# Kernel tuning notes

Measured on AMD Instinct MI355X. Metric: run time of the kernel, lower is better.

## Reference

```python
import jax, jax.numpy as jnp
import numpy as np

B, N, D_NODE, D_EDGE, D_GRAPH = 2, 1024, 128, 16, 128
MID, OUT = 64, 128


def _linear_params(key, fan_in, fan_out):
    # haiku Linear default: truncated-normal(stddev=1/sqrt(fan_in)) weight, zero bias
    w = jax.random.normal(key, (fan_in, fan_out), dtype=jnp.float32) / np.sqrt(fan_in)
    b = jnp.zeros((fan_out,), dtype=jnp.float32)
    return w, b


def setup_inputs() -> dict:
    key = jax.random.key(0)
    ks = jax.random.split(key, 12)
    features = jax.random.normal(ks[0], (B, N, D_NODE), dtype=jnp.float32)
    e_features = jax.random.normal(ks[1], (B, N, N, D_EDGE), dtype=jnp.float32)
    g_features = jax.random.normal(ks[2], (B, D_GRAPH), dtype=jnp.float32)
    adj = jax.random.randint(ks[3], (B, N, N), 0, 2).astype(jnp.float32)
    # ensure self-loops so every row has at least one valid neighbor
    adj = jnp.maximum(adj, jnp.eye(N, dtype=jnp.float32)[None])
    Wm, bm = _linear_params(ks[4], D_NODE, OUT)
    Wskip, bskip = _linear_params(ks[5], D_NODE, OUT)
    W1, b1 = _linear_params(ks[6], D_NODE, MID)
    W2, b2 = _linear_params(ks[7], D_NODE, MID)
    We, be = _linear_params(ks[8], D_EDGE, MID)
    Wg, bg = _linear_params(ks[9], D_GRAPH, MID)
    Wa, ba = _linear_params(ks[10], MID, 1)
    return dict(features=features, e_features=e_features, g_features=g_features,
                adj=adj, Wm=Wm, bm=bm, Wskip=Wskip, bskip=bskip,
                W1=W1, b1=b1, W2=W2, b2=b2, We=We, be=be, Wg=Wg, bg=bg,
                Wa=Wa, ba=ba)


def reference(features, e_features, g_features, adj,
              Wm, bm, Wskip, bskip, W1, b1, W2, b2, We, be, Wg, bg, Wa, ba):
    # bias mask: 0 where edge exists, -1e9 where not
    bias_mat = (adj - 1.0) * 1e9  # (b,n,n)

    values = features @ Wm + bm          # (b,n,out)
    pre_att_1 = features @ W1 + b1       # (b,n,mid) -> per-target j
    pre_att_2 = features @ W2 + b2       # (b,n,mid) -> per-source i
    pre_att_e = e_features @ We + be     # (b,n,n,mid)
    pre_att_g = g_features @ Wg + bg     # (b,mid)

    # pre_att[b,i,j] = p1[b,j] + p2[b,i] + pe[b,i,j] + pg[b]
    pre_att = (pre_att_1[:, None, :, :] + pre_att_2[:, :, None, :]
               + pre_att_e + pre_att_g[:, None, None, :])  # (b,n,n,mid)

    logits = jnp.squeeze(jax.nn.leaky_relu(pre_att) @ Wa + ba, axis=-1)  # (b,n,n)
    coefs = jax.nn.softmax(logits + bias_mat, axis=-1)                   # (b,n,n)

    ret = jnp.matmul(coefs, values)       # (b,n,out)
    ret = ret + (features @ Wskip + bskip)  # residual
    return jax.nn.relu(ret)               # activation=relu
```

## Files before the change

### kernel.cpp

```cpp
#include <hip/hip_runtime.h>
#include <hip/hip_bf16.h>
#include <cstdint>

#define B_   2
#define N_   1024
#define DN_  128
#define DE_  16
#define DG_  128
#define MID_ 64
#define OUT_ 128
#define TI_  2
#define PR_ROWS 4

typedef short bf16x8 __attribute__((ext_vector_type(8)));
typedef float f32x4  __attribute__((ext_vector_type(4)));

__device__ inline short f2bf(float f) {
    union { float f; unsigned u; } v; v.f = f;
    unsigned r = v.u + 0x7FFFu + ((v.u >> 16) & 1u);
    return (short)(unsigned short)(r >> 16);
}

__device__ inline unsigned pk2(float lo, float hi) {
    union { __hip_bfloat162 h; unsigned u; } p;
    p.h = __float22bfloat162_rn(make_float2(lo, hi));
    return p.u;
}

__global__ void __launch_bounds__(384) prep_all(
    const float* __restrict__ features, const float* __restrict__ g_features,
    const float* __restrict__ Wm, const float* __restrict__ bm,
    const float* __restrict__ Wskip, const float* __restrict__ bskip,
    const float* __restrict__ W1, const float* __restrict__ b1,
    const float* __restrict__ W2, const float* __restrict__ b2,
    const float* __restrict__ We, const float* __restrict__ be,
    const float* __restrict__ Wg, const float* __restrict__ bg,
    float* __restrict__ values, float* __restrict__ skipo,
    float* __restrict__ P1x, float* __restrict__ p2,
    float* __restrict__ pg, short* __restrict__ We_frag)
{
    const int t   = threadIdx.x;
    const int blk = blockIdx.x;

    if (blk == 512) {
        for (int e = t; e < 4 * 64 * 8; e += 384) {
            const int c    = e >> 9;
            const int lane = (e >> 3) & 63;
            const int j    = e & 7;
            const int quad = lane >> 4, s = lane & 15;
            short v = 0;
            if (quad < 2) v = f2bf(We[(quad * 8 + j) * MID_ + c * 16 + s]);
            We_frag[e] = v;
        }
        return;
    }
    if (blk == 513) {
        if (t < MID_) {
            float a0 = bg[t], a1 = bg[t];
            for (int k = 0; k < DG_; ++k) {
                const float w = Wg[k * MID_ + t];
                a0 += g_features[k] * w;
                a1 += g_features[DG_ + k] * w;
            }
            pg[t] = a0; pg[MID_ + t] = a1;
        }
        return;
    }

    const int r0 = blk * PR_ROWS;
    __shared__ float feat[PR_ROWS][DN_];
    for (int idx = t; idx < PR_ROWS * DN_; idx += 384)
        feat[idx >> 7][idx & 127] = features[(size_t)r0 * DN_ + idx];
    __syncthreads();

    const float* W; int c, stride; float base; float* outp; int ostride;
    if (t < 128) {
        W = Wm;    c = t;       stride = OUT_; base = bm[c];
        outp = values + (size_t)r0 * OUT_ + c; ostride = OUT_;
    } else if (t < 256) {
        W = Wskip; c = t - 128; stride = OUT_; base = bskip[c];
        outp = skipo + (size_t)r0 * OUT_ + c;  ostride = OUT_;
    } else if (t < 320) {
        W = W1;    c = t - 256; stride = MID_; base = b1[c] + be[c];
        outp = P1x + (size_t)r0 * MID_ + c;    ostride = MID_;
    } else {
        W = W2;    c = t - 320; stride = MID_; base = b2[c];
        outp = p2 + (size_t)r0 * MID_ + c;     ostride = MID_;
    }

    float acc[PR_ROWS] = {};
    for (int k = 0; k < DN_; ++k) {
        const float w = W[k * stride + c];
        #pragma unroll
        for (int q = 0; q < PR_ROWS; ++q) acc[q] += feat[q][k] * w;
    }
    #pragma unroll
    for (int q = 0; q < PR_ROWS; ++q) outp[q * ostride] = acc[q] + base;
}

__global__ void __launch_bounds__(256, 4) gat_main(
    const float* __restrict__ e_features, const float* __restrict__ adj,
    const short* __restrict__ We_frag, const float* __restrict__ Wa,
    const float* __restrict__ values, const float* __restrict__ skipo,
    const float* __restrict__ P1x, const float* __restrict__ p2,
    const float* __restrict__ pg, float* __restrict__ out)
{
    const int t    = threadIdx.x;
    const int wv   = t >> 6;
    const int l    = t & 63;
    const int quad = l >> 4;
    const int s    = l & 15;
    const int r    = blockIdx.x;
    const int b    = (r >> 2) & 1;
    const int i0   = (((r >> 3) << 2) | (r & 3)) * TI_;

    __shared__ float lgP[TI_][N_];
    __shared__ float redv[4][16][20];
    __shared__ float sinv[TI_];
    __shared__ float pmax[4];
    __shared__ float psum[4];

    bf16x8 bfr[4];
    float  wa_r[4], p2i[TI_][4];
    #pragma unroll
    for (int c = 0; c < 4; ++c) {
        bfr[c]  = *(const bf16x8*)&We_frag[(c * 64 + l) * 8];
        wa_r[c] = Wa[c * 16 + s];
        const float pgc = pg[b * MID_ + c * 16 + s];
        #pragma unroll
        for (int ii = 0; ii < TI_; ++ii)
            p2i[ii][c] = p2[((size_t)(b * N_ + i0 + ii)) * MID_ + c * 16 + s] + pgc;
    }
    const size_t erow0 = (size_t)(b * N_ + i0) * N_;

    float4 eA[TI_][2];
    if (quad < 2) {
        #pragma unroll
        for (int ii = 0; ii < TI_; ++ii) {
            const float* ep = &e_features[(erow0 + (size_t)ii * N_ + wv * 16 + s) * DE_ + quad * 8];
            eA[ii][0] = *(const float4*)ep;
            eA[ii][1] = *(const float4*)(ep + 4);
        }
    }
    for (int it = 0; it < 16; ++it) {
        const int tile = wv + it * 4;
        const int j0   = tile * 16;

        unsigned af[TI_][4];
        #pragma unroll
        for (int ii = 0; ii < TI_; ++ii) {
            if (quad < 2) {
                af[ii][0] = pk2(eA[ii][0].x, eA[ii][0].y);
                af[ii][1] = pk2(eA[ii][0].z, eA[ii][0].w);
                af[ii][2] = pk2(eA[ii][1].x, eA[ii][1].y);
                af[ii][3] = pk2(eA[ii][1].z, eA[ii][1].w);
            } else {
                af[ii][0] = af[ii][1] = af[ii][2] = af[ii][3] = 0u;
            }
        }
        if (it < 15) {
            const int jn = (tile + 4) * 16;
            if (quad < 2) {
                #pragma unroll
                for (int ii = 0; ii < TI_; ++ii) {
                    const float* ep = &e_features[(erow0 + (size_t)ii * N_ + jn + s) * DE_ + quad * 8];
                    eA[ii][0] = *(const float4*)ep;
                    eA[ii][1] = *(const float4*)(ep + 4);
                }
            }
        }
        float base[4][4];
        {
            const float* pb = &P1x[((size_t)(b * N_) + j0 + quad * 4) * MID_ + s];
            #pragma unroll
            for (int c = 0; c < 4; ++c)
                #pragma unroll
                for (int rr = 0; rr < 4; ++rr)
                    base[c][rr] = pb[rr * MID_ + c * 16];
        }
        #pragma unroll
        for (int ii = 0; ii < TI_; ++ii) {
            union { unsigned u[4]; bf16x8 v; } a;
            a.u[0] = af[ii][0]; a.u[1] = af[ii][1];
            a.u[2] = af[ii][2]; a.u[3] = af[ii][3];
            f32x4 acc[4];
            #pragma unroll
            for (int c = 0; c < 4; ++c) {
                acc[c] = (f32x4){0.f, 0.f, 0.f, 0.f};
                acc[c] = __builtin_amdgcn_mfma_f32_16x16x32_bf16(a.v, bfr[c], acc[c], 0, 0, 0);
            }
            float tt[4];
            #pragma unroll
            for (int rr = 0; rr < 4; ++rr) {
                float x0 = acc[0][rr] + base[0][rr] + p2i[ii][0];
                float x1 = acc[1][rr] + base[1][rr] + p2i[ii][1];
                float x2 = acc[2][rr] + base[2][rr] + p2i[ii][2];
                float x3 = acc[3][rr] + base[3][rr] + p2i[ii][3];
                x0 = fmaxf(x0, 0.01f * x0);
                x1 = fmaxf(x1, 0.01f * x1);
                x2 = fmaxf(x2, 0.01f * x2);
                x3 = fmaxf(x3, 0.01f * x3);
                tt[rr] = x0 * wa_r[0] + x1 * wa_r[1] + x2 * wa_r[2] + x3 * wa_r[3];
            }
            #pragma unroll
            for (int o = 1; o < 16; o <<= 1) {
                tt[0] += __shfl_xor(tt[0], o);
                tt[1] += __shfl_xor(tt[1], o);
                tt[2] += __shfl_xor(tt[2], o);
                tt[3] += __shfl_xor(tt[3], o);
            }
            if (s < 4) lgP[ii][j0 + quad * 4 + s] = tt[s];
        }
    }
    __syncthreads();

    {
        const int rw = wv & 1, h = wv >> 1;
        const int c0 = h * 512 + l * 4;
        const size_t arb = (size_t)(b * N_ + i0 + rw) * N_;
        float4 lv[2], av[2];
        #pragma unroll
        for (int q = 0; q < 2; ++q) {
            lv[q] = *(const float4*)&lgP[rw][c0 + 256 * q];
            av[q] = *(const float4*)&adj[arb + c0 + 256 * q];
        }
        const float NEG = -3.4e38f;
        float m = NEG;
        #pragma unroll
        for (int q = 0; q < 2; ++q) {
            m = fmaxf(m, av[q].x > 0.f ? lv[q].x : NEG);
            m = fmaxf(m, av[q].y > 0.f ? lv[q].y : NEG);
            m = fmaxf(m, av[q].z > 0.f ? lv[q].z : NEG);
            m = fmaxf(m, av[q].w > 0.f ? lv[q].w : NEG);
        }
        #pragma unroll
        for (int o = 1; o < 64; o <<= 1) m = fmaxf(m, __shfl_xor(m, o));
        if (l == 0) pmax[wv] = m;
        __syncthreads();
        m = fmaxf(pmax[rw], pmax[2 + rw]);
        float sum = 0.f;
        #pragma unroll
        for (int q = 0; q < 2; ++q) {
            float4 e4;
            e4.x = av[q].x > 0.f ? __expf(lv[q].x - m) : 0.f;
            e4.y = av[q].y > 0.f ? __expf(lv[q].y - m) : 0.f;
            e4.z = av[q].z > 0.f ? __expf(lv[q].z - m) : 0.f;
            e4.w = av[q].w > 0.f ? __expf(lv[q].w - m) : 0.f;
            *(float4*)&lgP[rw][c0 + 256 * q] = e4;
            sum += (e4.x + e4.y) + (e4.z + e4.w);
        }
        #pragma unroll
        for (int o = 1; o < 64; o <<= 1) sum += __shfl_xor(sum, o);
        if (l == 0) psum[wv] = sum;
        __syncthreads();
        if (t < TI_) sinv[t] = 1.0f / (psum[t] + psum[t + 2]);
    }

    const int cg = l & 15, jp = l >> 4, ch0 = cg * 8;
    float acc[TI_][8] = {};
    const float* vb = values + (size_t)b * N_ * OUT_ + ch0;
    for (int k = 0; k < 64; ++k) {
        const int j = wv * 4 + jp + k * 16;
        float cw[TI_];
        #pragma unroll
        for (int ii = 0; ii < TI_; ++ii) cw[ii] = lgP[ii][j];
        const float* vp = vb + (size_t)j * OUT_;
        const float4 v0 = *(const float4*)vp;
        const float4 v1 = *(const float4*)(vp + 4);
        const float vv[8] = {v0.x, v0.y, v0.z, v0.w, v1.x, v1.y, v1.z, v1.w};
        #pragma unroll
        for (int ii = 0; ii < TI_; ++ii)
            #pragma unroll
            for (int kk = 0; kk < 8; ++kk)
                acc[ii][kk] += cw[ii] * vv[kk];
    }
    #pragma unroll
    for (int ii = 0; ii < TI_; ++ii)
        #pragma unroll
        for (int kk = 0; kk < 8; ++kk) {
            acc[ii][kk] += __shfl_xor(acc[ii][kk], 16);
            acc[ii][kk] += __shfl_xor(acc[ii][kk], 32);
        }
    if (l < 16) {
        #pragma unroll
        for (int ii = 0; ii < TI_; ++ii)
            #pragma unroll
            for (int q = 0; q < 2; ++q) {
                float4 w4 = make_float4(acc[ii][q * 4], acc[ii][q * 4 + 1],
                                        acc[ii][q * 4 + 2], acc[ii][q * 4 + 3]);
                *(float4*)&redv[wv][l][ii * 8 + q * 4] = w4;
            }
    }
    __syncthreads();
    {
        const int ch = t & 127, g = ch >> 3, kk = ch & 7;
        const int ii = t >> 7;
        float sum = redv[0][g][ii * 8 + kk];
        #pragma unroll
        for (int w = 1; w < 4; ++w) sum += redv[w][g][ii * 8 + kk];
        const size_t ob = ((size_t)(b * N_ + i0 + ii)) * OUT_ + ch;
        out[ob] = fmaxf(sum * sinv[ii] + skipo[ob], 0.f);
    }
}

extern "C" void kernel_launch(void* const* d_in, const int* in_sizes, int n_in,
                              void* d_out, int out_size, void* d_ws, size_t ws_size,
                              hipStream_t stream) {
    const float* features   = (const float*)d_in[0];
    const float* e_features = (const float*)d_in[1];
    const float* g_features = (const float*)d_in[2];
    const float* adj        = (const float*)d_in[3];
    const float* Wm    = (const float*)d_in[4];
    const float* bm    = (const float*)d_in[5];
    const float* Wskip = (const float*)d_in[6];
    const float* bskip = (const float*)d_in[7];
    const float* W1    = (const float*)d_in[8];
    const float* b1    = (const float*)d_in[9];
    const float* W2    = (const float*)d_in[10];
    const float* b2    = (const float*)d_in[11];
    const float* We    = (const float*)d_in[12];
    const float* be    = (const float*)d_in[13];
    const float* Wg    = (const float*)d_in[14];
    const float* bg    = (const float*)d_in[15];
    const float* Wa    = (const float*)d_in[16];
    float* out = (float*)d_out;

    float* ws      = (float*)d_ws;
    float* values  = ws;
    float* skipo   = ws + 262144;
    float* P1x     = ws + 524288;
    float* p2      = ws + 655360;
    float* pg      = ws + 786432;
    short* We_frag = (short*)(ws + 786560);

    prep_all<<<B_ * N_ / PR_ROWS + 2, 384, 0, stream>>>(
        features, g_features, Wm, bm, Wskip, bskip, W1, b1, W2, b2,
        We, be, Wg, bg, values, skipo, P1x, p2, pg, We_frag);
    gat_main<<<B_ * N_ / TI_, 256, 0, stream>>>(
        e_features, adj, We_frag, Wa, values, skipo, P1x, p2, pg, out);
}
```

Baseline: 290.3 us.

## Split fused GAT kernel into logits and attention kernels with doubled grid

The single fused kernel becomes two. A logits kernel, launched with twice as many blocks each covering half the j range, writes the attention logits to a global workspace. A separate attention kernel then reads them back for the softmax and the aggregation. The bias sum (P1 + p2 + pg) is also folded into the MFMA accumulator input, which removes the post-MFMA adds. The aim is more parallelism and occupancy on the e_features-bound phase, at the cost of an extra launch and an 8 MB round trip of logits through global memory.

```diff
diff --git a/kernel.cpp b/kernel.cpp
--- a/kernel.cpp
+++ b/kernel.cpp
@@ -98,12 +98,11 @@
     for (int q = 0; q < PR_ROWS; ++q) outp[q * ostride] = acc[q] + base;
 }
 
-__global__ void __launch_bounds__(256, 4) gat_main(
-    const float* __restrict__ e_features, const float* __restrict__ adj,
-    const short* __restrict__ We_frag, const float* __restrict__ Wa,
-    const float* __restrict__ values, const float* __restrict__ skipo,
-    const float* __restrict__ P1x, const float* __restrict__ p2,
-    const float* __restrict__ pg, float* __restrict__ out)
+__global__ void __launch_bounds__(256) k_logits(
+    const float* __restrict__ e_features, const short* __restrict__ We_frag,
+    const float* __restrict__ Wa, const float* __restrict__ P1x,
+    const float* __restrict__ p2, const float* __restrict__ pg,
+    float* __restrict__ lg)
 {
     const int t    = threadIdx.x;
     const int wv   = t >> 6;
@@ -111,14 +110,10 @@
     const int quad = l >> 4;
     const int s    = l & 15;
     const int r    = blockIdx.x;
-    const int b    = (r >> 2) & 1;
-    const int i0   = (((r >> 3) << 2) | (r & 3)) * TI_;
-
-    __shared__ float lgP[TI_][N_];
-    __shared__ float redv[4][16][20];
-    __shared__ float sinv[TI_];
-    __shared__ float pmax[4];
-    __shared__ float psum[4];
+    const int jb   = r & 1;
+    const int ri   = r >> 1;
+    const int b    = ri >> 9;
+    const int i0   = (ri & 511) * TI_;
 
     bf16x8 bfr[4];
     float  wa_r[4], p2i[TI_][4];
@@ -132,18 +127,19 @@
             p2i[ii][c] = p2[((size_t)(b * N_ + i0 + ii)) * MID_ + c * 16 + s] + pgc;
     }
     const size_t erow0 = (size_t)(b * N_ + i0) * N_;
+    const int jt0 = jb * 32;
 
     float4 eA[TI_][2];
     if (quad < 2) {
         #pragma unroll
         for (int ii = 0; ii < TI_; ++ii) {
-            const float* ep = &e_features[(erow0 + (size_t)ii * N_ + wv * 16 + s) * DE_ + quad * 8];
+            const float* ep = &e_features[(erow0 + (size_t)ii * N_ + (jt0 + wv) * 16 + s) * DE_ + quad * 8];
             eA[ii][0] = *(const float4*)ep;
             eA[ii][1] = *(const float4*)(ep + 4);
         }
     }
-    for (int it = 0; it < 16; ++it) {
-        const int tile = wv + it * 4;
+    for (int it = 0; it < 8; ++it) {
+        const int tile = jt0 + wv + it * 4;
         const int j0   = tile * 16;
 
         unsigned af[TI_][4];
@@ -158,25 +154,23 @@
                 af[ii][0] = af[ii][1] = af[ii][2] = af[ii][3] = 0u;
             }
         }
-        if (it < 15) {
+        if (it < 7 && quad < 2) {
             const int jn = (tile + 4) * 16;
-            if (quad < 2) {
-                #pragma unroll
-                for (int ii = 0; ii < TI_; ++ii) {
-                    const float* ep = &e_features[(erow0 + (size_t)ii * N_ + jn + s) * DE_ + quad * 8];
-                    eA[ii][0] = *(const float4*)ep;
-                    eA[ii][1] = *(const float4*)(ep + 4);
-                }
-            }
-        }
-        float base[4][4];
+            #pragma unroll
+            for (int ii = 0; ii < TI_; ++ii) {
+                const float* ep = &e_features[(erow0 + (size_t)ii * N_ + jn + s) * DE_ + quad * 8];
+                eA[ii][0] = *(const float4*)ep;
+                eA[ii][1] = *(const float4*)(ep + 4);
+            }
+        }
+        float bse[4][4];
         {
             const float* pb = &P1x[((size_t)(b * N_) + j0 + quad * 4) * MID_ + s];
             #pragma unroll
             for (int c = 0; c < 4; ++c)
                 #pragma unroll
                 for (int rr = 0; rr < 4; ++rr)
-                    base[c][rr] = pb[rr * MID_ + c * 16];
+                    bse[c][rr] = pb[rr * MID_ + c * 16];
         }
         #pragma unroll
         for (int ii = 0; ii < TI_; ++ii) {
@@ -186,16 +180,17 @@
             f32x4 acc[4];
             #pragma unroll
             for (int c = 0; c < 4; ++c) {
-                acc[c] = (f32x4){0.f, 0.f, 0.f, 0.f};
-                acc[c] = __builtin_amdgcn_mfma_f32_16x16x32_bf16(a.v, bfr[c], acc[c], 0, 0, 0);
+                f32x4 cin;
+                cin[0] = bse[c][0] + p2i[ii][c];
+                cin[1] = bse[c][1] + p2i[ii][c];
+                cin[2] = bse[c][2] + p2i[ii][c];
+                cin[3] = bse[c][3] + p2i[ii][c];
+                acc[c] = __builtin_amdgcn_mfma_f32_16x16x32_bf16(a.v, bfr[c], cin, 0, 0, 0);
             }
             float tt[4];
             #pragma unroll
             for (int rr = 0; rr < 4; ++rr) {
-                float x0 = acc[0][rr] + base[0][rr] + p2i[ii][0];
-                float x1 = acc[1][rr] + base[1][rr] + p2i[ii][1];
-                float x2 = acc[2][rr] + base[2][rr] + p2i[ii][2];
-                float x3 = acc[3][rr] + base[3][rr] + p2i[ii][3];
+                float x0 = acc[0][rr], x1 = acc[1][rr], x2 = acc[2][rr], x3 = acc[3][rr];
                 x0 = fmaxf(x0, 0.01f * x0);
                 x1 = fmaxf(x1, 0.01f * x1);
                 x2 = fmaxf(x2, 0.01f * x2);
@@ -209,19 +204,39 @@
                 tt[2] += __shfl_xor(tt[2], o);
                 tt[3] += __shfl_xor(tt[3], o);
             }
-            if (s < 4) lgP[ii][j0 + quad * 4 + s] = tt[s];
-        }
-    }
-    __syncthreads();
+            if (s < 4)
+                lg[((size_t)(b * N_ + i0 + ii)) * N_ + j0 + quad * 4 + s] = tt[s];
+        }
+    }
+}
+
+__global__ void __launch_bounds__(256) k_attn(
+    const float* __restrict__ lg, const float* __restrict__ adj,
+    const float* __restrict__ values, const float* __restrict__ skipo,
+    float* __restrict__ out)
+{
+    const int t  = threadIdx.x;
+    const int wv = t >> 6;
+    const int l  = t & 63;
+    const int r  = blockIdx.x;
+    const int b  = (r >> 2) & 1;
+    const int i0 = (((r >> 3) << 2) | (r & 3)) * TI_;
+
+    __shared__ float lgP[TI_][N_];
+    __shared__ float redv[4][16][20];
+    __shared__ float sinv[TI_];
+    __shared__ float pmax[4];
+    __shared__ float psum[4];
 
     {
         const int rw = wv & 1, h = wv >> 1;
         const int c0 = h * 512 + l * 4;
-        const size_t arb = (size_t)(b * N_ + i0 + rw) * N_;
+        const float* lrow = &lg[(size_t)(b * N_ + i0 + rw) * N_];
+        const size_t arb  = (size_t)(b * N_ + i0 + rw) * N_;
         float4 lv[2], av[2];
         #pragma unroll
         for (int q = 0; q < 2; ++q) {
-            lv[q] = *(const float4*)&lgP[rw][c0 + 256 * q];
+            lv[q] = *(const float4*)&lrow[c0 + 256 * q];
             av[q] = *(const float4*)&adj[arb + c0 + 256 * q];
         }
         const float NEG = -3.4e38f;
@@ -332,10 +347,13 @@
     float* p2      = ws + 655360;
     float* pg      = ws + 786432;
     short* We_frag = (short*)(ws + 786560);
+    float* lg      = ws + 787584;
 
     prep_all<<<B_ * N_ / PR_ROWS + 2, 384, 0, stream>>>(
         features, g_features, Wm, bm, Wskip, bskip, W1, b1, W2, b2,
         We, be, Wg, bg, values, skipo, P1x, p2, pg, We_frag);
-    gat_main<<<B_ * N_ / TI_, 256, 0, stream>>>(
-        e_features, adj, We_frag, Wa, values, skipo, P1x, p2, pg, out);
-}
+    k_logits<<<B_ * N_ / TI_ * 2, 256, 0, stream>>>(
+        e_features, We_frag, Wa, P1x, p2, pg, lg);
+    k_attn<<<B_ * N_ / TI_, 256, 0, stream>>>(
+        lg, adj, values, skipo, out);
+}
```

Measured after the change: 307.3 us. +5.9%, slower.
